# Kernel tuning notes

Measured on AMD Instinct MI355X. Metric: run time of the kernel, lower is better.

## Reference

```python
import jax, jax.numpy as jnp
import numpy as np

B, HIMG, WIMG = 8, 24, 24
WIDTH, NCH, CW = 1024, 8, 128
NHEADS, HD = 8, 16
HALF = HD // 2
NFREQ, VOCAB, NCLS = 32, 256, 10
HIDDEN = 4096
EPS = 1e-6
LAMBDA_INIT = 0.8 - 0.6 * float(np.exp(-0.3 * 0.0))  # layer_idx = 0


def rmsnorm(x, w, eps=EPS):
    return x * jax.lax.rsqrt(jnp.mean(x * x, axis=-1, keepdims=True) + eps) * w


def causal_attn(q, k, v, scale):
    # q,k: [B,H,L,d2], v: [B,H,L,D]
    L = q.shape[2]
    scores = jnp.einsum('bhqd,bhkd->bhqk', q, k) * scale
    mask = jnp.tril(jnp.ones((L, L), dtype=bool))
    scores = jnp.where(mask, scores, -jnp.inf)
    return jnp.einsum('bhqk,bhkd->bhqd', jax.nn.softmax(scores, axis=-1), v)


def diff_attn(h, qkv_w, qkv_b, qn_w, kn_w, hn_w, lq1, lk1, lq2, lk2, ow, ob):
    Bb, L, C = h.shape
    qkv = jax.nn.silu(h @ qkv_w + qkv_b).reshape(Bb, L, 3, NHEADS, HD)
    q, k, v = qkv[:, :, 0], qkv[:, :, 1], qkv[:, :, 2]
    t = lambda a: a.transpose(0, 2, 1, 3)  # [B,L,H,d] -> [B,H,L,d]
    q1 = t(rmsnorm(q[..., :HALF], qn_w)); q2 = t(rmsnorm(q[..., HALF:], qn_w))
    k1 = t(rmsnorm(k[..., :HALF], kn_w)); k2 = t(rmsnorm(k[..., HALF:], kn_w))
    v = t(v)
    lam = jnp.exp(jnp.dot(lq1, lk1)) - jnp.exp(jnp.dot(lq2, lk2)) + LAMBDA_INIT
    scale = 1.0 / np.sqrt(HALF)
    out1 = causal_attn(q1, k1, v, scale)
    out2 = causal_attn(q2, k2, v, scale)
    diff = rmsnorm(out1 - lam * out2, hn_w) * (1.0 - LAMBDA_INIT)
    out = diff.transpose(0, 2, 1, 3).reshape(Bb, L, C)
    return jax.nn.silu(out @ ow + ob)


def setup_inputs() -> dict:
    key = jax.random.key(0)
    ks = iter(jax.random.split(key, 64))
    n = lambda shape, s=0.02: jax.random.normal(next(ks), shape, jnp.float32) * s
    return dict(
        x=jax.random.uniform(next(ks), (B, HIMG, WIMG), jnp.float32),
        top_k=4,
        pixel_embed=n((VOCAB, WIDTH)),
        freq_h=n((NFREQ,), 0.1), freq_w=n((NFREQ,), 0.1),
        phase_h=jnp.zeros((NFREQ,), jnp.float32), phase_w=jnp.zeros((NFREQ,), jnp.float32),
        pos_proj_w=n((4 * NFREQ, WIDTH)), pos_proj_b=jnp.zeros((WIDTH,), jnp.float32),
        embed_norm_w=jnp.ones((WIDTH,), jnp.float32),
        se_w1=n((WIDTH, WIDTH // 4)), se_b1=jnp.zeros((WIDTH // 4,), jnp.float32),
        se_w2=n((WIDTH // 4, WIDTH)), se_b2=jnp.zeros((WIDTH,), jnp.float32),
        mix_norm_w=jnp.ones((WIDTH,), jnp.float32),
        mlp_w1=n((WIDTH, HIDDEN)), mlp_b1=jnp.zeros((HIDDEN,), jnp.float32),
        mlp_w2=n((HIDDEN, WIDTH)), mlp_b2=jnp.zeros((WIDTH,), jnp.float32),
        mlp_norm_w=jnp.ones((WIDTH,), jnp.float32),
        router_w=n((WIDTH, NCH)), router_b=jnp.zeros((NCH,), jnp.float32),
        qkv_w=n((NCH, CW, 3 * CW)), qkv_b=jnp.zeros((NCH, 3 * CW), jnp.float32),
        q_norm_w=jnp.ones((NCH, HALF), jnp.float32), k_norm_w=jnp.ones((NCH, HALF), jnp.float32),
        head_norm_w=jnp.ones((NCH, HD), jnp.float32),
        lam_q1=n((NCH, HALF), 0.1), lam_k1=n((NCH, HALF), 0.1),
        lam_q2=n((NCH, HALF), 0.1), lam_k2=n((NCH, HALF), 0.1),
        out_w=n((NCH, CW, CW)), out_b=jnp.zeros((NCH, CW), jnp.float32),
        seg_norm_w=jnp.ones((NCH, CW), jnp.float32),
        head_w=n((WIDTH, NCLS)), head_b=jnp.zeros((NCLS,), jnp.float32),
    )


def reference(x, top_k, pixel_embed, freq_h, freq_w, phase_h, phase_w, pos_proj_w,
              pos_proj_b, embed_norm_w, se_w1, se_b1, se_w2, se_b2, mix_norm_w,
              mlp_w1, mlp_b1, mlp_w2, mlp_b2, mlp_norm_w, router_w, router_b,
              qkv_w, qkv_b, q_norm_w, k_norm_w, head_norm_w, lam_q1, lam_k1,
              lam_q2, lam_k2, out_w, out_b, seg_norm_w, head_w, head_b):
    Bb, H, W = x.shape
    L = H * W
    # LearnedSinusoidal2DEmbed
    hp = jnp.arange(H, dtype=jnp.float32) / H
    wp = jnp.arange(W, dtype=jnp.float32) / W
    fh = jax.nn.softplus(freq_h) * 10.0
    fw = jax.nn.softplus(freq_w) * 10.0
    ha = hp[:, None] * fh + phase_h          # [H, NFREQ]
    wa = wp[:, None] * fw + phase_w
    h_enc = jnp.concatenate([jnp.sin(ha), jnp.cos(ha)], -1)
    w_enc = jnp.concatenate([jnp.sin(wa), jnp.cos(wa)], -1)
    pos = jnp.concatenate([jnp.broadcast_to(h_enc[:, None], (H, W, 2 * NFREQ)),
                           jnp.broadcast_to(w_enc[None, :], (H, W, 2 * NFREQ))], -1)
    pos = pos @ pos_proj_w + pos_proj_b      # [H, W, WIDTH]
    xi = jnp.clip((x * 255.0).astype(jnp.int32), 0, 255).reshape(Bb, L)
    h = pixel_embed[xi] + pos.reshape(1, L, WIDTH)
    h = rmsnorm(h, embed_norm_w)
    # ChannelMixer: SE + RMSNorm residual, MLP residual, top-k router
    s = jnp.mean(h, axis=1)
    s = jax.nn.sigmoid(jax.nn.silu(s @ se_w1 + se_b1) @ se_w2 + se_b2)
    h = h + rmsnorm(h * s[:, None, :] - h, mix_norm_w)
    h = h + rmsnorm(jax.nn.silu(h @ mlp_w1 + mlp_b1) @ mlp_w2 + mlp_b2, mlp_norm_w)
    logits_r = jnp.mean(h, axis=1) @ router_w + router_b   # [B, NCH]
    tv, ti = jax.lax.top_k(logits_r, top_k)
    rw = jnp.zeros_like(logits_r).at[jnp.arange(Bb)[:, None], ti].set(jax.nn.softmax(tv, axis=-1))
    # ChannelSegment: per-channel differential attention expert, routed
    outs = []
    for i in range(NCH):
        hi = h[..., i * CW:(i + 1) * CW]
        o = diff_attn(hi, qkv_w[i], qkv_b[i], q_norm_w[i], k_norm_w[i], head_norm_w[i],
                      lam_q1[i], lam_k1[i], lam_q2[i], lam_k2[i], out_w[i], out_b[i])
        hi = hi + rmsnorm(o, seg_norm_w[i])
        outs.append(hi * rw[:, i][:, None, None])
    h = jnp.concatenate(outs, axis=-1)
    # classifier head
    return jnp.mean(h, axis=1) @ head_w + head_b
```

## Files before the change

### kernel.cpp

```cpp
#include <hip/hip_runtime.h>
#include <math.h>

typedef __bf16 bf16;
typedef __bf16 bf16x8 __attribute__((ext_vector_type(8)));
typedef __bf16 bf16x4 __attribute__((ext_vector_type(4)));
typedef __bf16 bf16x2 __attribute__((ext_vector_type(2)));
typedef float f32x4 __attribute__((ext_vector_type(4)));
typedef short s16x4 __attribute__((ext_vector_type(4)));

constexpr int Bsz = 8, HIMG = 24, WIMG = 24;
constexpr int Lq = 576;
constexpr int WIDTH = 1024, NCH = 8, CW = 128;
constexpr int NHEADS = 8, HD = 16, HALF = 8;
constexpr float EPS = 1e-6f;
constexpr float LAMINIT = 0.2f;
constexpr float QSCALE_E = 0.35355339059327373f * 1.4426950408889634f;
constexpr int ROWS = Bsz * Lq;
constexpr long PSTRIDE = 4718592;

__device__ __forceinline__ float fexp2(float x) {
#if __has_builtin(__builtin_amdgcn_exp2f)
  return __builtin_amdgcn_exp2f(x);
#else
  return exp2f(x);
#endif
}

constexpr size_t B_HB    = 0;
constexpr size_t B_G2B   = B_HB    + 9437184;
constexpr size_t B_ENCB  = B_G2B   + 9437184;
constexpr size_t B_POSWT = B_ENCB  + 163840;
constexpr size_t B_QKVWT = B_POSWT + 262144;
constexpr size_t B_OWT   = B_QKVWT + 786432;
constexpr size_t B_SE    = B_OWT   + 262144;
constexpr size_t B_T1    = B_SE    + 32768;
constexpr size_t B_MP    = B_T1    + 8192;
constexpr size_t B_RW    = B_MP    + 524288;
constexpr size_t B_LAM   = B_RW    + 256;
constexpr size_t B_POOL  = B_LAM   + 256;
constexpr size_t WS_BIG  = B_POOL + 8388608 + 8388608 + 37748736;
constexpr size_t WS_BIG2 = WS_BIG + 9437184;
constexpr size_t WS_BIG3 = WS_BIG + 4 * 9437184;

__device__ __forceinline__ float blockReduceSum256(float v, float* red) {
  #pragma unroll
  for (int off = 32; off; off >>= 1) v += __shfl_down(v, off, 64);
  int lane = threadIdx.x & 63, wid = threadIdx.x >> 6;
  if (lane == 0) red[wid] = v;
  __syncthreads();
  float total = 0.f;
  #pragma unroll
  for (int i = 0; i < 4; i++) total += red[i];
  return total;
}
__device__ __forceinline__ float silu(float x) { return x / (1.f + __expf(-x)); }

__device__ __forceinline__ void gl16(const bf16* g, bf16* l) {
  __builtin_amdgcn_global_load_lds(
      (const __attribute__((address_space(1))) void*)g,
      (__attribute__((address_space(3))) void*)l, 16, 0, 0);
}

__device__ __forceinline__ f32x4 mfma16(bf16x4 a, bf16x4 b, f32x4 c) {
#if __has_builtin(__builtin_amdgcn_mfma_f32_16x16x16bf16_1k)
  union { bf16x4 h; s16x4 s; } ua, ub;
  ua.h = a; ub.h = b;
  return __builtin_amdgcn_mfma_f32_16x16x16bf16_1k(ua.s, ub.s, c, 0, 0, 0);
#else
  f32x4 d = c;
  asm volatile("v_mfma_f32_16x16x16_bf16 %0, %1, %2, %0"
               : "+v"(d) : "v"(a), "v"(b));
  return d;
#endif
}

__device__ __forceinline__ void tcast_tile(const float* __restrict__ W,
    bf16* __restrict__ Wt, int K, int N, long zo, int bx, int by) {
  __shared__ float t[32][33];
  int n0 = bx * 32, k0 = by * 32;
  int tid = threadIdx.x;
  int r = tid >> 3, c4 = (tid & 7) * 4;
  const float4 v = *(const float4*)(W + zo + (long)(k0 + r) * N + n0 + c4);
  t[c4 + 0][r] = v.x; t[c4 + 1][r] = v.y; t[c4 + 2][r] = v.z; t[c4 + 3][r] = v.w;
  __syncthreads();
  bf16* dst = Wt + zo + (long)(n0 + r) * K + k0 + c4;
  bf16x4 o4;
  o4[0] = (bf16)t[r][c4 + 0]; o4[1] = (bf16)t[r][c4 + 1];
  o4[2] = (bf16)t[r][c4 + 2]; o4[3] = (bf16)t[r][c4 + 3];
  *(bf16x4*)dst = o4;
}

__global__ __launch_bounds__(256) void k_tcast_all(
    const float* __restrict__ w1, const float* __restrict__ w2,
    const float* __restrict__ posw, const float* __restrict__ qkvw,
    const float* __restrict__ outw,
    bf16* __restrict__ W1T, bf16* __restrict__ W2T, bf16* __restrict__ POSWT,
    bf16* __restrict__ QKVWT, bf16* __restrict__ OWT) {
  int bid = blockIdx.x;
  if (bid < 4096) {
    tcast_tile(w1, W1T, 1024, 4096, 0, bid % 128, bid / 128);
  } else if (bid < 8192) {
    int t = bid - 4096;
    tcast_tile(w2, W2T, 4096, 1024, 0, t % 32, t / 32);
  } else if (bid < 8320) {
    int t = bid - 8192;
    tcast_tile(posw, POSWT, 128, 1024, 0, t % 32, t / 32);
  } else if (bid < 8704) {
    int t = bid - 8320;
    int z = t / 48; t -= z * 48;
    tcast_tile(qkvw, QKVWT, 128, 384, (long)z * 49152, t % 12, t / 12);
  } else {
    int t = bid - 8704;
    int z = t / 16; t -= z * 16;
    tcast_tile(outw, OWT, 128, 128, (long)z * 16384, t % 4, t / 4);
  }
}

__global__ void k_enc_b(const float* __restrict__ fh, const float* __restrict__ fw,
                        const float* __restrict__ ph, const float* __restrict__ pw,
                        bf16* __restrict__ enc) {
  int idx = blockIdx.x * blockDim.x + threadIdx.x;
  if (idx >= Lq * 128) return;
  int l = idx >> 7, c = idx & 127;
  int hh = l / WIMG, ww = l % WIMG;
  float v;
  if (c < 64) {
    int f = c & 31;
    float fr = log1pf(__expf(fh[f])) * 10.f;
    float a = (hh / (float)HIMG) * fr + ph[f];
    v = (c < 32) ? sinf(a) : cosf(a);
  } else {
    int f = c & 31;
    float fr = log1pf(__expf(fw[f])) * 10.f;
    float a = (ww / (float)WIMG) * fr + pw[f];
    v = (c < 96) ? sinf(a) : cosf(a);
  }
  enc[idx] = (bf16)v;
}

template <int ACT, int OUTBF, int SWZ>
__global__ __launch_bounds__(256) void gemm_bt(
    const bf16* __restrict__ A, int lda, long aZs,
    const bf16* __restrict__ Bt, int ldb, long bZs,
    const float* __restrict__ bias, int biasZs,
    void* __restrict__ Cv, int ldc, long cZs,
    int M, int N, int K) {
  __shared__ bf16 As[128 * 32];
  __shared__ bf16 Bs[128 * 32];
  int tid = threadIdx.x;
  int m0, n0, z;
  if constexpr (SWZ == 0) {
    m0 = blockIdx.y * 128; n0 = blockIdx.x * 128; z = blockIdx.z;
  } else if constexpr (SWZ == 1) {
    int lid = blockIdx.x;
    int xcd = lid & 7, idx = lid >> 3;
    int j = idx & 15, G = xcd + 8 * (idx >> 4);
    m0 = (G % 36) * 128; n0 = ((G / 36) * 16 + j) * 128; z = 0;
  } else {
    int lid = blockIdx.x;
    int xcd = lid & 7, idx = lid >> 3;
    int n = idx & 7, G = xcd + 8 * (idx >> 3);
    m0 = (G % 36) * 128; n0 = n * 128; z = G / 36;
  }
  const bf16* Ab = A + (long)z * aZs;
  const bf16* Bb = Bt + (long)z * bZs;
  f32x4 acc[4][4] = {};
  int wv = tid >> 6, lane = tid & 63;
  int wrow = (wv >> 1) * 64, wcol = (wv & 1) * 64;
  int lm = lane & 15, lq = lane >> 4;
  const bf16* ag = Ab + (long)(m0 + (tid >> 2)) * lda + (tid & 3) * 8;
  const bf16* bg = Bb + (long)(n0 + (tid >> 2)) * ldb + (tid & 3) * 8;
  bf16* asd = As + tid * 8;
  bf16* bsd = Bs + tid * 8;
  for (int k0 = 0; k0 < K; k0 += 32) {
    gl16(ag + k0, asd);
    gl16(ag + k0 + 64L * lda, asd + 2048);
    gl16(bg + k0, bsd);
    gl16(bg + k0 + 64L * ldb, bsd + 2048);
    __syncthreads();
    bf16x8 af[4], bfr[4];
    #pragma unroll
    for (int i = 0; i < 4; i++) {
      af[i]  = *(const bf16x8*)(As + (wrow + i * 16 + lm) * 32 + lq * 8);
      bfr[i] = *(const bf16x8*)(Bs + (wcol + i * 16 + lm) * 32 + lq * 8);
    }
    #pragma unroll
    for (int i = 0; i < 4; i++)
      #pragma unroll
      for (int j = 0; j < 4; j++)
        acc[i][j] = __builtin_amdgcn_mfma_f32_16x16x32_bf16(af[i], bfr[j], acc[i][j], 0, 0, 0);
    __syncthreads();
  }
  long cz = (long)z * cZs;
  const float* bz = bias ? bias + (long)z * biasZs : nullptr;
  #pragma unroll
  for (int i = 0; i < 4; i++) {
    int row = m0 + wrow + i * 16 + lq * 4;
    #pragma unroll
    for (int j = 0; j < 4; j++) {
      int col = n0 + wcol + j * 16 + lm;
      float bv = bz ? bz[col] : 0.f;
      #pragma unroll
      for (int r = 0; r < 4; r++) {
        float v = acc[i][j][r] + bv;
        if (ACT == 1) v = silu(v);
        long off = cz + (long)(row + r) * ldc + col;
        if (OUTBF) ((bf16*)Cv)[off] = (bf16)v;
        else       ((float*)Cv)[off] = v;
      }
    }
  }
}

template <int ACT>
__global__ __launch_bounds__(512) void gemm256(
    const bf16* __restrict__ A, int lda, long aZs,
    const bf16* __restrict__ Bt, int ldb, long bZs,
    const float* __restrict__ bias,
    bf16* __restrict__ C, int ldc, long cZs,
    int Mtiles, int Ntiles, int K) {
  __shared__ bf16 LDS[65536];
  const int tid = threadIdx.x;
  const int cpx = gridDim.x >> 3;
  const int wg = (blockIdx.x & 7) * cpx + (blockIdx.x >> 3);
  const int per_z = Mtiles * Ntiles;
  const int z = wg / per_z, rwg = wg % per_z;
  const int m0 = (rwg / Ntiles) * 256, n0 = (rwg % Ntiles) * 256;
  const bf16* Ab = A + (long)z * aZs;
  const bf16* Bb = Bt + (long)z * bZs;
  const int c0 = tid, c1 = tid + 512;
  const int sr0 = c0 >> 3, sc0 = ((c0 & 7) ^ (((sr0 >> 2) & 1) << 1)) * 8;
  const int sr1 = c1 >> 3, sc1 = ((c1 & 7) ^ (((sr1 >> 2) & 1) << 1)) * 8;
  const long a00 = (long)(m0 + sr0) * lda + sc0;
  const long a01 = (long)(m0 + sr1) * lda + sc1;
  const long a10 = (long)(m0 + 128 + sr0) * lda + sc0;
  const long a11 = (long)(m0 + 128 + sr1) * lda + sc1;
  const long b00 = (long)(n0 + sr0) * ldb + sc0;
  const long b01 = (long)(n0 + sr1) * ldb + sc1;
  const long b10 = (long)(n0 + 128 + sr0) * ldb + sc0;
  const long b11 = (long)(n0 + 128 + sr1) * ldb + sc1;
  const int d0 = c0 * 8, d1 = c1 * 8;
  auto stage = [&](int kt, int buf) {
    const bf16* Ak = Ab + kt * 64;
    const bf16* Bk = Bb + kt * 64;
    bf16* L = LDS + buf * 32768;
    gl16(Ak + a00, L + d0);         gl16(Ak + a01, L + d1);
    gl16(Ak + a10, L + 8192 + d0);  gl16(Ak + a11, L + 8192 + d1);
    gl16(Bk + b00, L + 16384 + d0); gl16(Bk + b01, L + 16384 + d1);
    gl16(Bk + b10, L + 24576 + d0); gl16(Bk + b11, L + 24576 + d1);
  };
  const int wv = tid >> 6, lane = tid & 63;
  const int wm = wv >> 2, wn = wv & 3;
  const int lm = lane & 15, lq = lane >> 4;
  const int swb = ((lm >> 2) & 1) << 1;
  const int abase = wm * 8192;
  const int bbase = 16384 + (wn >> 1) * 8192;
  const int brow0 = (wn & 1) * 64;
  const int kq0 = (lq ^ swb) * 8;
  const int kq1 = ((4 + lq) ^ swb) * 8;
  f32x4 acc[8][4] = {};
  bf16x8 afr[4][2], bfr[2][2];
  const int NT = K >> 6;
  stage(0, 0);
  asm volatile("s_waitcnt vmcnt(0)" ::: "memory");
  __builtin_amdgcn_s_barrier();
  for (int s = 0; s < NT; ++s) {
    const int bb = (s & 1) * 32768;
    const bf16* La = LDS + bb + abase + lm * 64;
    const bf16* Lb = LDS + bb + bbase + (brow0 + lm) * 64;
    #pragma unroll
    for (int f = 0; f < 4; f++) {
      afr[f][0] = *(const bf16x8*)(La + f * 1024 + kq0);
      afr[f][1] = *(const bf16x8*)(La + f * 1024 + kq1);
    }
    #pragma unroll
    for (int g = 0; g < 2; g++) {
      bfr[g][0] = *(const bf16x8*)(Lb + g * 1024 + kq0);
      bfr[g][1] = *(const bf16x8*)(Lb + g * 1024 + kq1);
    }
    if (s + 1 < NT) stage(s + 1, ((s & 1) ^ 1));
    __builtin_amdgcn_s_barrier();
    __builtin_amdgcn_s_setprio(1);
    #pragma unroll
    for (int f = 0; f < 4; f++)
      #pragma unroll
      for (int g = 0; g < 2; g++) {
        acc[f][g] = __builtin_amdgcn_mfma_f32_16x16x32_bf16(afr[f][0], bfr[g][0], acc[f][g], 0, 0, 0);
        acc[f][g] = __builtin_amdgcn_mfma_f32_16x16x32_bf16(afr[f][1], bfr[g][1], acc[f][g], 0, 0, 0);
      }
    __builtin_amdgcn_s_setprio(0);
    __builtin_amdgcn_s_barrier();
    #pragma unroll
    for (int g = 0; g < 2; g++) {
      bfr[g][0] = *(const bf16x8*)(Lb + 2048 + g * 1024 + kq0);
      bfr[g][1] = *(const bf16x8*)(Lb + 2048 + g * 1024 + kq1);
    }
    __builtin_amdgcn_s_barrier();
    __builtin_amdgcn_s_setprio(1);
    #pragma unroll
    for (int f = 0; f < 4; f++)
      #pragma unroll
      for (int g = 0; g < 2; g++) {
        acc[f][2 + g] = __builtin_amdgcn_mfma_f32_16x16x32_bf16(afr[f][0], bfr[g][0], acc[f][2 + g], 0, 0, 0);
        acc[f][2 + g] = __builtin_amdgcn_mfma_f32_16x16x32_bf16(afr[f][1], bfr[g][1], acc[f][2 + g], 0, 0, 0);
      }
    __builtin_amdgcn_s_setprio(0);
    __builtin_amdgcn_s_barrier();
    #pragma unroll
    for (int f = 0; f < 4; f++) {
      afr[f][0] = *(const bf16x8*)(La + 4096 + f * 1024 + kq0);
      afr[f][1] = *(const bf16x8*)(La + 4096 + f * 1024 + kq1);
    }
    __builtin_amdgcn_s_barrier();
    __builtin_amdgcn_s_setprio(1);
    #pragma unroll
    for (int f = 0; f < 4; f++)
      #pragma unroll
      for (int g = 0; g < 2; g++) {
        acc[4 + f][2 + g] = __builtin_amdgcn_mfma_f32_16x16x32_bf16(afr[f][0], bfr[g][0], acc[4 + f][2 + g], 0, 0, 0);
        acc[4 + f][2 + g] = __builtin_amdgcn_mfma_f32_16x16x32_bf16(afr[f][1], bfr[g][1], acc[4 + f][2 + g], 0, 0, 0);
      }
    __builtin_amdgcn_s_setprio(0);
    __builtin_amdgcn_s_barrier();
    #pragma unroll
    for (int g = 0; g < 2; g++) {
      bfr[g][0] = *(const bf16x8*)(Lb + g * 1024 + kq0);
      bfr[g][1] = *(const bf16x8*)(Lb + g * 1024 + kq1);
    }
    __builtin_amdgcn_s_barrier();
    __builtin_amdgcn_s_setprio(1);
    #pragma unroll
    for (int f = 0; f < 4; f++)
      #pragma unroll
      for (int g = 0; g < 2; g++) {
        acc[4 + f][g] = __builtin_amdgcn_mfma_f32_16x16x32_bf16(afr[f][0], bfr[g][0], acc[4 + f][g], 0, 0, 0);
        acc[4 + f][g] = __builtin_amdgcn_mfma_f32_16x16x32_bf16(afr[f][1], bfr[g][1], acc[4 + f][g], 0, 0, 0);
      }
    __builtin_amdgcn_s_setprio(0);
    if (s + 1 < NT) { asm volatile("s_waitcnt vmcnt(0)" ::: "memory"); }
    __builtin_amdgcn_s_barrier();
  }
  const long cz = (long)z * cZs;
  #pragma unroll
  for (int i = 0; i < 8; i++) {
    const int row = m0 + wm * 128 + (i >> 2) * 64 + (i & 3) * 16 + lq * 4;
    #pragma unroll
    for (int j = 0; j < 4; j++) {
      const int col = n0 + wn * 64 + (j >> 1) * 32 + (j & 1) * 16 + lm;
      const float bv = bias ? bias[col] : 0.f;
      #pragma unroll
      for (int rr = 0; rr < 4; rr++) {
        float v = acc[i][j][rr] + bv;
        if (ACT == 1) v = silu(v);
        C[cz + (long)(row + rr) * ldc + col] = (bf16)v;
      }
    }
  }
}

template <int ACT, int OUTBF, int ACC, int NORM>
__global__ __launch_bounds__(256) void gemm64(
    const bf16* __restrict__ A, int lda, long aZs,
    const bf16* __restrict__ Bt, int ldb, long bZs,
    const float* __restrict__ bias, int biasZs,
    void* __restrict__ Cv, int ldc, long cZs,
    int M, int N, int K,
    const float* __restrict__ qn, const float* __restrict__ kn) {
  __shared__ bf16 As[64 * 32];
  __shared__ bf16 Bs[128 * 32];
  int tid = threadIdx.x;
  int m0 = blockIdx.y * 64, n0 = blockIdx.x * 128;
  int z = blockIdx.z;
  const bf16* Ab = A + (long)z * aZs;
  const bf16* Bb = Bt + (long)z * bZs;
  f32x4 acc[4][2] = {};
  int wv = tid >> 6, lane = tid & 63;
  int lm = lane & 15, lq = lane >> 4;
  int wcol = wv * 32;
  const bf16* ag = Ab + (long)(m0 + (tid >> 2)) * lda + (tid & 3) * 8;
  const bf16* bg = Bb + (long)(n0 + (tid >> 2)) * ldb + (tid & 3) * 8;
  bf16* asd = As + tid * 8;
  bf16* bsd = Bs + tid * 8;
  for (int k0 = 0; k0 < K; k0 += 32) {
    gl16(ag + k0, asd);
    gl16(bg + k0, bsd);
    gl16(bg + k0 + 64L * ldb, bsd + 2048);
    __syncthreads();
    bf16x8 af[4], bfr[2];
    #pragma unroll
    for (int i = 0; i < 4; i++)
      af[i] = *(const bf16x8*)(As + (i * 16 + lm) * 32 + lq * 8);
    #pragma unroll
    for (int j = 0; j < 2; j++)
      bfr[j] = *(const bf16x8*)(Bs + (wcol + j * 16 + lm) * 32 + lq * 8);
    #pragma unroll
    for (int i = 0; i < 4; i++)
      #pragma unroll
      for (int j = 0; j < 2; j++)
        acc[i][j] = __builtin_amdgcn_mfma_f32_16x16x32_bf16(af[i], bfr[j], acc[i][j], 0, 0, 0);
    __syncthreads();
  }
  long cz = (long)z * cZs;
  const float* bz = bias ? bias + (long)z * biasZs : nullptr;
  if constexpr (NORM == 0) {
    #pragma unroll
    for (int i = 0; i < 4; i++) {
      int row = m0 + i * 16 + lq * 4;
      #pragma unroll
      for (int j = 0; j < 2; j++) {
        int col = n0 + wcol + j * 16 + lm;
        float bv = bz ? bz[col] : 0.f;
        #pragma unroll
        for (int r = 0; r < 4; r++) {
          float v = acc[i][j][r] + bv;
          long off = cz + (long)(row + r) * ldc + col;
          if (ACC) v += (float)((bf16*)Cv)[off];
          if (ACT == 1) v = silu(v);
          if (OUTBF) ((bf16*)Cv)[off] = (bf16)v;
          else       ((float*)Cv)[off] = v;
        }
      }
    }
  } else {
    int nsec = blockIdx.x;
    bool don = nsec < 2;
    float wnv = 1.f;
    if (nsec == 0) wnv = qn[z * 8 + (lm & 7)] * QSCALE_E;
    else if (nsec == 1) wnv = kn[z * 8 + (lm & 7)];
    #pragma unroll
    for (int i = 0; i < 4; i++) {
      int row = m0 + i * 16 + lq * 4;
      #pragma unroll
      for (int j = 0; j < 2; j++) {
        int col = n0 + wcol + j * 16 + lm;
        float bv = bz ? bz[col] : 0.f;
        #pragma unroll
        for (int r = 0; r < 4; r++) {
          float v = acc[i][j][r] + bv;
          if (ACT == 1) v = silu(v);
          float s = v * v;
          s += __shfl_xor(s, 1);
          s += __shfl_xor(s, 2);
          s += __shfl_xor(s, 4);
          if (don) v = v * rsqrtf(s * 0.125f + EPS) * wnv;
          ((bf16*)Cv)[cz + (long)(row + r) * ldc + col] = (bf16)v;
        }
      }
    }
  }
}

__global__ __launch_bounds__(256) void k_embed(const float* __restrict__ x,
    const float* __restrict__ emb, const float* __restrict__ pos,
    const float* __restrict__ nw, bf16* __restrict__ h) {
  __shared__ float red[4];
  int row = blockIdx.x;
  int l = row % Lq;
  int xi = (int)(x[row] * 255.f);
  xi = min(max(xi, 0), 255);
  const float* er = emb + (long)xi * WIDTH;
  const float* pr = pos + (long)l * WIDTH;
  int c0 = threadIdx.x * 4;
  float v[4]; float ss = 0.f;
  #pragma unroll
  for (int i = 0; i < 4; i++) { v[i] = er[c0 + i] + pr[c0 + i]; ss += v[i] * v[i]; }
  ss = blockReduceSum256(ss, red);
  float r = rsqrtf(ss / WIDTH + EPS);
  bf16* hr = h + (long)row * WIDTH;
  #pragma unroll
  for (int i = 0; i < 4; i++) hr[c0 + i] = (bf16)(v[i] * r * nw[c0 + i]);
}

__global__ void k_meanl_p(const bf16* __restrict__ h, float* __restrict__ part) {
  int lp = blockIdx.x, b = blockIdx.y, t = threadIdx.x;
  const bf16* p = h + ((long)b * Lq + (long)lp * 36) * WIDTH + t * 4;
  float a0 = 0, a1 = 0, a2 = 0, a3 = 0;
  for (int l = 0; l < 36; l++) {
    bf16x4 v = *(const bf16x4*)(p + (long)l * WIDTH);
    a0 += (float)v[0]; a1 += (float)v[1]; a2 += (float)v[2]; a3 += (float)v[3];
  }
  float* dst = part + ((long)b * 16 + lp) * WIDTH + t * 4;
  dst[0] = a0; dst[1] = a1; dst[2] = a2; dst[3] = a3;
}

__global__ __launch_bounds__(256) void k_se1(const float* __restrict__ part,
    const float* __restrict__ w1, const float* __restrict__ b1,
    float* __restrict__ t1) {
  __shared__ float sv[1024];
  __shared__ float red[256];
  int jb = blockIdx.x, b = blockIdx.y, t = threadIdx.x;
  for (int c = t; c < 1024; c += 256) {
    float a = 0.f;
    #pragma unroll
    for (int lp = 0; lp < 16; lp++) a += part[((long)b * 16 + lp) * 1024 + c];
    sv[c] = a * (1.f / 576.f);
  }
  __syncthreads();
  int j = t & 7, pt = t >> 3;
  int j0 = jb * 8;
  float acc = 0.f;
  int c0 = pt * 32;
  #pragma unroll 8
  for (int c = c0; c < c0 + 32; c++) acc += sv[c] * w1[c * 256 + j0 + j];
  red[t] = acc;
  __syncthreads();
  if (t < 8) {
    float a = b1[j0 + t];
    #pragma unroll
    for (int p = 0; p < 32; p++) a += red[p * 8 + t];
    t1[b * 256 + j0 + t] = silu(a);
  }
}

__global__ __launch_bounds__(256) void k_se2(const float* __restrict__ t1,
    const float* __restrict__ w2, const float* __restrict__ b2,
    float* __restrict__ s) {
  __shared__ float red[256];
  int jb = blockIdx.x, b = blockIdx.y, t = threadIdx.x;
  int j = t & 31, pt = t >> 5;
  int j0 = jb * 32;
  const float* tb = t1 + b * 256;
  float acc = 0.f;
  int c0 = pt * 32;
  #pragma unroll 8
  for (int c = c0; c < c0 + 32; c++) acc += tb[c] * w2[c * 1024 + j0 + j];
  red[t] = acc;
  __syncthreads();
  if (t < 32) {
    float a = b2[j0 + t];
    #pragma unroll
    for (int p = 0; p < 8; p++) a += red[p * 32 + t];
    s[b * 1024 + j0 + t] = 1.f / (1.f + __expf(-a));
  }
}

__global__ __launch_bounds__(256) void k_mix_b(bf16* __restrict__ h,
    const float* __restrict__ s, const float* __restrict__ mw) {
  __shared__ float red[4];
  int row = blockIdx.x;
  int b = row / Lq;
  bf16* hr = h + (long)row * WIDTH;
  const float* sb = s + b * WIDTH;
  int c0 = threadIdx.x * 4;
  float hv[4], y[4]; float ss = 0.f;
  #pragma unroll
  for (int i = 0; i < 4; i++) {
    hv[i] = (float)hr[c0 + i];
    y[i] = hv[i] * (sb[c0 + i] - 1.f); ss += y[i] * y[i];
  }
  ss = blockReduceSum256(ss, red);
  float r = rsqrtf(ss / WIDTH + EPS);
  #pragma unroll
  for (int i = 0; i < 4; i++) hr[c0 + i] = (bf16)(hv[i] + y[i] * r * mw[c0 + i]);
}

__global__ __launch_bounds__(256) void k_addnorm_b(bf16* __restrict__ h,
    const bf16* __restrict__ g, const float* __restrict__ mw) {
  __shared__ float red[4];
  int row = blockIdx.x;
  bf16* hr = h + (long)row * WIDTH;
  const bf16* gr = g + (long)row * WIDTH;
  int c0 = threadIdx.x * 4;
  float y[4]; float ss = 0.f;
  #pragma unroll
  for (int i = 0; i < 4; i++) { y[i] = (float)gr[c0 + i]; ss += y[i] * y[i]; }
  ss = blockReduceSum256(ss, red);
  float r = rsqrtf(ss / WIDTH + EPS);
  #pragma unroll
  for (int i = 0; i < 4; i++)
    hr[c0 + i] = (bf16)((float)hr[c0 + i] + y[i] * r * mw[c0 + i]);
}

__global__ __launch_bounds__(256) void k_addnorm2(bf16* __restrict__ h,
    const bf16* __restrict__ p0, const bf16* __restrict__ p1,
    const float* __restrict__ b2, const float* __restrict__ mw) {
  __shared__ float red[4];
  int row = blockIdx.x;
  bf16* hr = h + (long)row * WIDTH;
  const bf16* g0 = p0 + (long)row * WIDTH;
  const bf16* g1 = p1 + (long)row * WIDTH;
  int c0 = threadIdx.x * 4;
  float y[4]; float ss = 0.f;
  #pragma unroll
  for (int i = 0; i < 4; i++) {
    y[i] = (float)g0[c0 + i] + (float)g1[c0 + i] + b2[c0 + i];
    ss += y[i] * y[i];
  }
  ss = blockReduceSum256(ss, red);
  float r = rsqrtf(ss / WIDTH + EPS);
  #pragma unroll
  for (int i = 0; i < 4; i++)
    hr[c0 + i] = (bf16)((float)hr[c0 + i] + y[i] * r * mw[c0 + i]);
}

__global__ __launch_bounds__(256) void k_addnorm4(bf16* __restrict__ h,
    const bf16* __restrict__ parts, const float* __restrict__ b2,
    const float* __restrict__ mw) {
  __shared__ float red[4];
  int row = blockIdx.x;
  bf16* hr = h + (long)row * WIDTH;
  const bf16* g0 = parts + (long)row * WIDTH;
  int c0 = threadIdx.x * 4;
  float y[4]; float ss = 0.f;
  #pragma unroll
  for (int i = 0; i < 4; i++) {
    float a = b2[c0 + i];
    #pragma unroll
    for (int p = 0; p < 4; p++) a += (float)g0[(long)p * PSTRIDE + c0 + i];
    y[i] = a; ss += a * a;
  }
  ss = blockReduceSum256(ss, red);
  float r = rsqrtf(ss / WIDTH + EPS);
  #pragma unroll
  for (int i = 0; i < 4; i++)
    hr[c0 + i] = (bf16)((float)hr[c0 + i] + y[i] * r * mw[c0 + i]);
}

__global__ __launch_bounds__(256) void k_router(const float* __restrict__ part,
    const float* __restrict__ rwgt, const float* __restrict__ rb,
    const float* __restrict__ lq1, const float* __restrict__ lk1,
    const float* __restrict__ lq2, const float* __restrict__ lk2,
    float* __restrict__ rw, float* __restrict__ lam) {
  __shared__ float sv[1024];
  __shared__ float red[256];
  __shared__ float lg[8];
  int b = blockIdx.x, t = threadIdx.x;
  for (int c = t; c < 1024; c += 256) {
    float a = 0.f;
    #pragma unroll
    for (int lp = 0; lp < 16; lp++) a += part[((long)b * 16 + lp) * 1024 + c];
    sv[c] = a * (1.f / 576.f);
  }
  __syncthreads();
  int j = t & 7, pt = t >> 3;
  float acc = 0.f;
  int c0 = pt * 32;
  #pragma unroll 8
  for (int c = c0; c < c0 + 32; c++) acc += sv[c] * rwgt[c * 8 + j];
  red[t] = acc;
  __syncthreads();
  if (t < 8) {
    float a = rb[t];
    for (int p = 0; p < 32; p++) a += red[p * 8 + t];
    lg[t] = a;
  }
  __syncthreads();
  if (t == 0) {
    float v[8]; bool sel[8];
    #pragma unroll
    for (int i = 0; i < 8; i++) { v[i] = lg[i]; sel[i] = false; }
    int idxs[4]; float vals[4];
    for (int s = 0; s < 4; s++) {
      int bi = -1; float bv = -1e30f;
      for (int i = 0; i < 8; i++) if (!sel[i] && v[i] > bv) { bv = v[i]; bi = i; }
      sel[bi] = true; idxs[s] = bi; vals[s] = bv;
    }
    float m = vals[0], den = 0.f, e[4];
    for (int s = 0; s < 4; s++) { e[s] = __expf(vals[s] - m); den += e[s]; }
    for (int i = 0; i < 8; i++) rw[b * 8 + i] = 0.f;
    for (int s = 0; s < 4; s++) rw[b * 8 + idxs[s]] = e[s] / den;
  }
  if (b == 0 && t >= 8 && t < 16) {
    int c = t - 8;
    float d1 = 0.f, d2 = 0.f;
    for (int i = 0; i < 8; i++) {
      d1 += lq1[c * 8 + i] * lk1[c * 8 + i];
      d2 += lq2[c * 8 + i] * lk2[c * 8 + i];
    }
    lam[c] = __expf(d1) - __expf(d2) + LAMINIT;
  }
}

__global__ __launch_bounds__(256) void k_attn_mfma(
    const bf16* __restrict__ qkv, const float* __restrict__ lam,
    const float* __restrict__ hnw, bf16* __restrict__ dc) {
  __shared__ bf16 Ks[576 * 16];
  __shared__ bf16 Vt[16 * 584];
  int tid = threadIdx.x;
  int slice = blockIdx.x; int zc = slice >> 3, b = slice & 7;
  int head = blockIdx.z;
  const bf16* qkvb = qkv + ((long)zc * ROWS + (long)b * Lq) * 384;
  for (int i = tid; i < 1152; i += 256) {
    int row = i >> 1, hf = i & 1;
    gl16(qkvb + (long)row * 384 + 128 + head * 16 + hf * 8, Ks + i * 8);
  }
  for (int i = tid; i < 1152; i += 256) {
    int row = i >> 1, dh = i & 1;
    bf16x8 v = *(const bf16x8*)(qkvb + (long)row * 384 + 256 + head * 16 + dh * 8);
    #pragma unroll
    for (int j = 0; j < 8; j++) Vt[(dh * 8 + j) * 584 + row] = v[j];
  }
  __syncthreads();
  int wv = tid >> 6, lane = tid & 63;
  int lm = lane & 15, lq = lane >> 4;
  float lamv = lam[zc];
  float hwv[4];
  #pragma unroll
  for (int r = 0; r < 4; r++) hwv[r] = hnw[zc * 16 + lq * 4 + r] * (1.f - LAMINIT);
  const bf16 one = (bf16)1.0f;
  const bf16x4 ONES = {one, one, one, one};
  int u = blockIdx.y * 4 + wv;
  int prA, prB, prC;
  if (u < 6) { prA = u + 2; prB = 17 - u; prC = -1; }
  else       { int v2 = u - 6; prA = v2; prB = 8 + v2; prC = 11 - v2; }
  for (int pi = 0; pi < 3; pi++) {
    int pr = (pi == 0) ? prA : (pi == 1) ? prB : prC;
    if (pr < 0) continue;
    bf16x8 bq0[2] = {{}, {}}, bq1[2] = {{}, {}};
    if (lq < 2) {
      #pragma unroll
      for (int tile = 0; tile < 2; tile++) {
        bf16x8 t8 = *(const bf16x8*)(
            qkvb + (long)(pr * 32 + tile * 16 + lm) * 384 + head * 16 + lq * 8);
        if (lq == 0) bq0[tile] = t8; else bq1[tile] = t8;
      }
    }
    f32x4 o[2][2] = {};
    f32x4 dacc[2][2] = {};
    for (int kc = 0; kc <= pr; kc++) {
      f32x4 sT[2][2][2] = {};
      #pragma unroll
      for (int t = 0; t < 2; t++) {
        bf16x8 aK = {};
        if (lq < 2) aK = *(const bf16x8*)(Ks + (kc * 32 + t * 16 + lm) * 16 + lq * 8);
        #pragma unroll
        for (int tile = 0; tile < 2; tile++) {
          sT[t][tile][0] = __builtin_amdgcn_mfma_f32_16x16x32_bf16(aK, bq0[tile], sT[t][tile][0], 0, 0, 0);
          sT[t][tile][1] = __builtin_amdgcn_mfma_f32_16x16x32_bf16(aK, bq1[tile], sT[t][tile][1], 0, 0, 0);
        }
      }
      bool diag = (kc == pr);
      #pragma unroll
      for (int t = 0; t < 2; t++) {
        bf16x4 aV = *(const bf16x4*)(Vt + lm * 584 + kc * 32 + t * 16 + lq * 4);
        #pragma unroll
        for (int tile = 0; tile < 2; tile++) {
          if (diag && tile == 0 && t == 1) continue;
          bool masked = diag && (tile == t);
          #pragma unroll
          for (int h2 = 0; h2 < 2; h2++) {
            bf16x4 pb;
            #pragma unroll
            for (int r = 0; r < 4; r++) {
              float ev = fexp2(sT[t][tile][h2][r]);
              if (masked && (lq * 4 + r > lm)) ev = 0.f;
              pb[r] = (bf16)ev;
            }
            dacc[tile][h2] = mfma16(ONES, pb, dacc[tile][h2]);
            o[tile][h2] = mfma16(aV, pb, o[tile][h2]);
          }
        }
      }
    }
    #pragma unroll
    for (int tile = 0; tile < 2; tile++) {
      float inv1 = 1.f / dacc[tile][0][0];
      float inv2 = lamv / dacc[tile][1][0];
      float dff[4]; float ss = 0.f;
      #pragma unroll
      for (int r = 0; r < 4; r++) {
        dff[r] = o[tile][0][r] * inv1 - o[tile][1][r] * inv2;
        ss += dff[r] * dff[r];
      }
      ss += __shfl_xor(ss, 16);
      ss += __shfl_xor(ss, 32);
      float rr = rsqrtf(ss * 0.0625f + EPS);
      bf16x4 outp;
      #pragma unroll
      for (int r = 0; r < 4; r++) outp[r] = (bf16)(dff[r] * rr * hwv[r]);
      long rowg = (long)zc * ROWS + (long)b * Lq + pr * 32 + tile * 16 + lm;
      *(bf16x4*)(dc + rowg * 128 + head * 16 + lq * 4) = outp;
    }
  }
}

__global__ __launch_bounds__(64) void k_segpool(const bf16* __restrict__ h,
    const bf16* __restrict__ op, const float* __restrict__ segw,
    const float* __restrict__ rw, float* __restrict__ part) {
  int lp = blockIdx.x, b = blockIdx.y, ch = blockIdx.z;
  int t = threadIdx.x;
  int c0 = t * 2;
  float w0 = segw[ch * 128 + c0], w1 = segw[ch * 128 + c0 + 1];
  float rwv = rw[b * 8 + ch];
  float a0 = 0.f, a1 = 0.f;
  for (int l = 0; l < 36; l++) {
    int row = b * Lq + lp * 36 + l;
    const bf16* oprow = op + (long)ch * ROWS * CW + (long)row * CW;
    bf16x2 yv = *(const bf16x2*)(oprow + c0);
    float y0 = (float)yv[0], y1 = (float)yv[1];
    float ss = y0 * y0 + y1 * y1;
    #pragma unroll
    for (int m = 1; m < 64; m <<= 1) ss += __shfl_xor(ss, m);
    float r = rsqrtf(ss * (1.f / 128.f) + EPS);
    bf16x2 hv = *(const bf16x2*)(h + (long)row * WIDTH + ch * 128 + c0);
    a0 += ((float)hv[0] + y0 * r * w0) * rwv;
    a1 += ((float)hv[1] + y1 * r * w1) * rwv;
  }
  float* dst = part + ((long)b * 16 + lp) * 1024 + ch * 128 + c0;
  dst[0] = a0; dst[1] = a1;
}

__global__ __launch_bounds__(256) void k_head(const float* __restrict__ part,
    const float* __restrict__ hw, const float* __restrict__ hb, float* __restrict__ out) {
  __shared__ float pool[1024];
  __shared__ float red[256];
  int b = blockIdx.x, t = threadIdx.x;
  for (int c = t; c < 1024; c += 256) {
    float a = 0.f;
    #pragma unroll
    for (int lp = 0; lp < 16; lp++) a += part[((long)b * 16 + lp) * 1024 + c];
    pool[c] = a * (1.f / 576.f);
  }
  __syncthreads();
  int j = t & 15, pt = t >> 4;
  float acc = 0.f;
  if (j < 10)
    for (int c = pt * 64; c < pt * 64 + 64; c++)
      acc += pool[c] * hw[c * 10 + j];
  red[t] = acc;
  __syncthreads();
  if (t < 10) {
    float a = hb[t];
    for (int p = 0; p < 16; p++) a += red[p * 16 + t];
    out[b * 10 + t] = a;
  }
}

extern "C" void kernel_launch(void* const* d_in, const int* in_sizes, int n_in,
                              void* d_out, int out_size, void* d_ws, size_t ws_size,
                              hipStream_t stream) {
  const float* x          = (const float*)d_in[0];
  const float* pixel_embed= (const float*)d_in[2];
  const float* freq_h     = (const float*)d_in[3];
  const float* freq_w     = (const float*)d_in[4];
  const float* phase_h    = (const float*)d_in[5];
  const float* phase_w    = (const float*)d_in[6];
  const float* pos_proj_w = (const float*)d_in[7];
  const float* pos_proj_b = (const float*)d_in[8];
  const float* embed_norm = (const float*)d_in[9];
  const float* se_w1      = (const float*)d_in[10];
  const float* se_b1      = (const float*)d_in[11];
  const float* se_w2      = (const float*)d_in[12];
  const float* se_b2      = (const float*)d_in[13];
  const float* mix_norm   = (const float*)d_in[14];
  const float* mlp_w1     = (const float*)d_in[15];
  const float* mlp_b1     = (const float*)d_in[16];
  const float* mlp_w2     = (const float*)d_in[17];
  const float* mlp_b2     = (const float*)d_in[18];
  const float* mlp_norm   = (const float*)d_in[19];
  const float* router_w   = (const float*)d_in[20];
  const float* router_b   = (const float*)d_in[21];
  const float* qkv_w      = (const float*)d_in[22];
  const float* qkv_b      = (const float*)d_in[23];
  const float* q_norm_w   = (const float*)d_in[24];
  const float* k_norm_w   = (const float*)d_in[25];
  const float* head_norm_w= (const float*)d_in[26];
  const float* lam_q1     = (const float*)d_in[27];
  const float* lam_k1     = (const float*)d_in[28];
  const float* lam_q2     = (const float*)d_in[29];
  const float* lam_k2     = (const float*)d_in[30];
  const float* out_w      = (const float*)d_in[31];
  const float* out_b      = (const float*)d_in[32];
  const float* seg_norm_w = (const float*)d_in[33];
  const float* head_w     = (const float*)d_in[34];
  const float* head_b     = (const float*)d_in[35];

  char* W = (char*)d_ws;
  bf16*  HB    = (bf16*)(W + B_HB);
  bf16*  G2B   = (bf16*)(W + B_G2B);
  float* POS   = (float*)(W + B_G2B);
  bf16*  ENCB  = (bf16*)(W + B_ENCB);
  bf16*  POSWT = (bf16*)(W + B_POSWT);
  bf16*  QKVWT = (bf16*)(W + B_QKVWT);
  bf16*  OWT   = (bf16*)(W + B_OWT);
  float* SE    = (float*)(W + B_SE);
  float* T1    = (float*)(W + B_T1);
  float* MP    = (float*)(W + B_MP);
  float* RW    = (float*)(W + B_RW);
  float* LAM   = (float*)(W + B_LAM);
  char*  P     = W + B_POOL;
  bf16*  W1T   = (bf16*)P;
  bf16*  W2T   = (bf16*)(P + 8388608);
  bf16*  HID   = (bf16*)(P + 16777216);
  bf16*  PARTS = (bf16*)(P + 16777216 + 37748736);
  bf16*  QKV   = (bf16*)P;
  bf16*  DC    = (bf16*)(P + 28311552);
  float* out   = (float*)d_out;
  const int tier = (ws_size >= WS_BIG3) ? 3 : (ws_size >= WS_BIG2) ? 2
                 : (ws_size >= WS_BIG) ? 1 : 0;

  k_tcast_all<<<8832, 256, 0, stream>>>(mlp_w1, mlp_w2, pos_proj_w, qkv_w, out_w,
                                        W1T, W2T, POSWT, QKVWT, OWT);
  k_enc_b<<<288, 256, 0, stream>>>(freq_h, freq_w, phase_h, phase_w, ENCB);
  gemm64<0, 0, 0, 0><<<dim3(8, 10, 1), 256, 0, stream>>>(
      ENCB, 128, 0, POSWT, 128, 0, pos_proj_b, 0, POS, 1024, 0, 640, 1024, 128,
      nullptr, nullptr);
  k_embed<<<ROWS, 256, 0, stream>>>(x, pixel_embed, POS, embed_norm, HB);
  k_meanl_p<<<dim3(16, 8), 256, 0, stream>>>(HB, MP);
  k_se1<<<dim3(32, 8), 256, 0, stream>>>(MP, se_w1, se_b1, T1);
  k_se2<<<dim3(32, 8), 256, 0, stream>>>(T1, se_w2, se_b2, SE);
  k_mix_b<<<ROWS, 256, 0, stream>>>(HB, SE, mix_norm);
  if (tier >= 1) {
    gemm256<1><<<256, 512, 0, stream>>>(
        HB, 1024, 0, W1T, 1024, 0, mlp_b1,
        HID, 4096, 0, 16, 16, 1024);
    gemm_bt<1, 1, 0><<<dim3(32, 4, 1), 256, 0, stream>>>(
        HB + 4096L * 1024, 1024, 0, W1T, 1024, 0, mlp_b1, 0,
        HID + 4096L * 4096, 4096, 0, 512, 4096, 1024);
    if (tier == 3) {
      gemm256<0><<<256, 512, 0, stream>>>(
          HID, 4096, 1024, W2T, 4096, 1024, nullptr,
          PARTS, 1024, PSTRIDE, 16, 4, 1024);
      gemm_bt<0, 1, 0><<<dim3(8, 4, 4), 256, 0, stream>>>(
          HID + 4096L * 4096, 4096, 1024, W2T, 4096, 1024, nullptr, 0,
          PARTS + 4096L * 1024, 1024, PSTRIDE, 512, 1024, 1024);
      k_addnorm4<<<ROWS, 256, 0, stream>>>(HB, PARTS, mlp_b2, mlp_norm);
    } else if (tier == 2) {
      gemm_bt<0, 1, 2><<<576, 256, 0, stream>>>(
          HID, 4096, 2048, W2T, 4096, 2048, nullptr, 0,
          G2B, 1024, (long)(PARTS - G2B), 4608, 1024, 2048);
      k_addnorm2<<<ROWS, 256, 0, stream>>>(HB, G2B, PARTS, mlp_b2, mlp_norm);
    } else {
      gemm64<0, 1, 0, 0><<<dim3(8, 72, 1), 256, 0, stream>>>(
          HID, 4096, 0, W2T, 4096, 0, mlp_b2, 0,
          G2B, 1024, 0, 4608, 1024, 4096, nullptr, nullptr);
      k_addnorm_b<<<ROWS, 256, 0, stream>>>(HB, G2B, mlp_norm);
    }
  } else {
    gemm_bt<1, 1, 0><<<dim3(16, 36, 1), 256, 0, stream>>>(
        HB, 1024, 0, W1T, 1024, 0, mlp_b1, 0, HID, 2048, 0, 4608, 2048, 1024);
    gemm64<0, 1, 0, 0><<<dim3(8, 72, 1), 256, 0, stream>>>(
        HID, 2048, 0, W2T, 4096, 0, mlp_b2, 0, G2B, 1024, 0, 4608, 1024, 2048,
        nullptr, nullptr);
    gemm_bt<1, 1, 0><<<dim3(16, 36, 1), 256, 0, stream>>>(
        HB, 1024, 0, W1T + 2048L * 1024, 1024, 0, mlp_b1 + 2048, 0, HID, 2048, 0,
        4608, 2048, 1024);
    gemm64<0, 1, 1, 0><<<dim3(8, 72, 1), 256, 0, stream>>>(
        HID, 2048, 0, W2T + 2048, 4096, 0, nullptr, 0, G2B, 1024, 0,
        4608, 1024, 2048, nullptr, nullptr);
    k_addnorm_b<<<ROWS, 256, 0, stream>>>(HB, G2B, mlp_norm);
  }
  k_meanl_p<<<dim3(16, 8), 256, 0, stream>>>(HB, MP);
  k_router<<<8, 256, 0, stream>>>(MP, router_w, router_b,
                                  lam_q1, lam_k1, lam_q2, lam_k2, RW, LAM);
  gemm64<1, 1, 0, 1><<<dim3(3, 72, 8), 256, 0, stream>>>(
      HB, 1024, CW, QKVWT, 128, 384 * 128, qkv_b, 384,
      QKV, 384, (long)ROWS * 384, ROWS, 384, 128, q_norm_w, k_norm_w);
  k_attn_mfma<<<dim3(64, 2, 8), 256, 0, stream>>>(QKV, LAM, head_norm_w, DC);
  gemm64<1, 1, 0, 0><<<dim3(1, 72, 8), 256, 0, stream>>>(
      DC, 128, (long)ROWS * 128, OWT, 128, 128 * 128, out_b, 128,
      DC, 128, (long)ROWS * 128, ROWS, 128, 128, nullptr, nullptr);
  k_segpool<<<dim3(16, 8, 8), 64, 0, stream>>>(HB, DC, seg_norm_w, RW, MP);
  k_head<<<8, 256, 0, stream>>>(MP, head_w, head_b, out);
}
```

Before: 456.2 us.

## Use full XOR LDS swizzle and drop intra-iteration barriers in gemm256

The LDS swizzle now XORs the 16-byte column chunk with the full row index (row & 7) instead of a single bit, aiming to spread fragment reads across more banks. The main loop now uses one __syncthreads per K-step and issues the next stage's global-to-LDS loads right after it. All A and B fragments for the step are held in separate registers, so the eight s_barrier calls between MFMA groups are gone. The cost is more VGPRs per thread, which may limit occupancy or cause spills. It also relies on __syncthreads draining the outstanding async LDS loads.

```diff
diff --git a/kernel.cpp b/kernel.cpp
--- a/kernel.cpp
+++ b/kernel.cpp
@@ -229,8 +229,8 @@
   const bf16* Ab = A + (long)z * aZs;
   const bf16* Bb = Bt + (long)z * bZs;
   const int c0 = tid, c1 = tid + 512;
-  const int sr0 = c0 >> 3, sc0 = ((c0 & 7) ^ (((sr0 >> 2) & 1) << 1)) * 8;
-  const int sr1 = c1 >> 3, sc1 = ((c1 & 7) ^ (((sr1 >> 2) & 1) << 1)) * 8;
+  const int sr0 = c0 >> 3, sc0 = ((c0 & 7) ^ (sr0 & 7)) * 8;
+  const int sr1 = c1 >> 3, sc1 = ((c1 & 7) ^ (sr1 & 7)) * 8;
   const long a00 = (long)(m0 + sr0) * lda + sc0;
   const long a01 = (long)(m0 + sr1) * lda + sc1;
   const long a10 = (long)(m0 + 128 + sr0) * lda + sc0;
@@ -252,93 +252,78 @@
   const int wv = tid >> 6, lane = tid & 63;
   const int wm = wv >> 2, wn = wv & 3;
   const int lm = lane & 15, lq = lane >> 4;
-  const int swb = ((lm >> 2) & 1) << 1;
+  const int sw = lm & 7;
   const int abase = wm * 8192;
   const int bbase = 16384 + (wn >> 1) * 8192;
   const int brow0 = (wn & 1) * 64;
-  const int kq0 = (lq ^ swb) * 8;
-  const int kq1 = ((4 + lq) ^ swb) * 8;
+  const int kq0 = (lq ^ sw) * 8;
+  const int kq1 = ((4 + lq) ^ sw) * 8;
   f32x4 acc[8][4] = {};
-  bf16x8 afr[4][2], bfr[2][2];
   const int NT = K >> 6;
   stage(0, 0);
-  asm volatile("s_waitcnt vmcnt(0)" ::: "memory");
-  __builtin_amdgcn_s_barrier();
   for (int s = 0; s < NT; ++s) {
+    __syncthreads();
+    if (s + 1 < NT) stage(s + 1, (s + 1) & 1);
     const int bb = (s & 1) * 32768;
     const bf16* La = LDS + bb + abase + lm * 64;
     const bf16* Lb = LDS + bb + bbase + (brow0 + lm) * 64;
+    bf16x8 a0[4][2], a1[4][2], b0[2][2], b1[2][2];
     #pragma unroll
     for (int f = 0; f < 4; f++) {
-      afr[f][0] = *(const bf16x8*)(La + f * 1024 + kq0);
-      afr[f][1] = *(const bf16x8*)(La + f * 1024 + kq1);
+      a0[f][0] = *(const bf16x8*)(La + f * 1024 + kq0);
+      a0[f][1] = *(const bf16x8*)(La + f * 1024 + kq1);
     }
     #pragma unroll
     for (int g = 0; g < 2; g++) {
-      bfr[g][0] = *(const bf16x8*)(Lb + g * 1024 + kq0);
-      bfr[g][1] = *(const bf16x8*)(Lb + g * 1024 + kq1);
-    }
-    if (s + 1 < NT) stage(s + 1, ((s & 1) ^ 1));
-    __builtin_amdgcn_s_barrier();
+      b0[g][0] = *(const bf16x8*)(Lb + g * 1024 + kq0);
+      b0[g][1] = *(const bf16x8*)(Lb + g * 1024 + kq1);
+    }
     __builtin_amdgcn_s_setprio(1);
     #pragma unroll
     for (int f = 0; f < 4; f++)
       #pragma unroll
       for (int g = 0; g < 2; g++) {
-        acc[f][g] = __builtin_amdgcn_mfma_f32_16x16x32_bf16(afr[f][0], bfr[g][0], acc[f][g], 0, 0, 0);
-        acc[f][g] = __builtin_amdgcn_mfma_f32_16x16x32_bf16(afr[f][1], bfr[g][1], acc[f][g], 0, 0, 0);
+        acc[f][g] = __builtin_amdgcn_mfma_f32_16x16x32_bf16(a0[f][0], b0[g][0], acc[f][g], 0, 0, 0);
+        acc[f][g] = __builtin_amdgcn_mfma_f32_16x16x32_bf16(a0[f][1], b0[g][1], acc[f][g], 0, 0, 0);
       }
     __builtin_amdgcn_s_setprio(0);
-    __builtin_amdgcn_s_barrier();
     #pragma unroll
     for (int g = 0; g < 2; g++) {
-      bfr[g][0] = *(const bf16x8*)(Lb + 2048 + g * 1024 + kq0);
-      bfr[g][1] = *(const bf16x8*)(Lb + 2048 + g * 1024 + kq1);
-    }
-    __builtin_amdgcn_s_barrier();
+      b1[g][0] = *(const bf16x8*)(Lb + 2048 + g * 1024 + kq0);
+      b1[g][1] = *(const bf16x8*)(Lb + 2048 + g * 1024 + kq1);
+    }
     __builtin_amdgcn_s_setprio(1);
     #pragma unroll
     for (int f = 0; f < 4; f++)
       #pragma unroll
       for (int g = 0; g < 2; g++) {
-        acc[f][2 + g] = __builtin_amdgcn_mfma_f32_16x16x32_bf16(afr[f][0], bfr[g][0], acc[f][2 + g], 0, 0, 0);
-        acc[f][2 + g] = __builtin_amdgcn_mfma_f32_16x16x32_bf16(afr[f][1], bfr[g][1], acc[f][2 + g], 0, 0, 0);
+        acc[f][2 + g] = __builtin_amdgcn_mfma_f32_16x16x32_bf16(a0[f][0], b1[g][0], acc[f][2 + g], 0, 0, 0);
+        acc[f][2 + g] = __builtin_amdgcn_mfma_f32_16x16x32_bf16(a0[f][1], b1[g][1], acc[f][2 + g], 0, 0, 0);
       }
     __builtin_amdgcn_s_setprio(0);
-    __builtin_amdgcn_s_barrier();
     #pragma unroll
     for (int f = 0; f < 4; f++) {
-      afr[f][0] = *(const bf16x8*)(La + 4096 + f * 1024 + kq0);
-      afr[f][1] = *(const bf16x8*)(La + 4096 + f * 1024 + kq1);
-    }
-    __builtin_amdgcn_s_barrier();
+      a1[f][0] = *(const bf16x8*)(La + 4096 + f * 1024 + kq0);
+      a1[f][1] = *(const bf16x8*)(La + 4096 + f * 1024 + kq1);
+    }
     __builtin_amdgcn_s_setprio(1);
     #pragma unroll
     for (int f = 0; f < 4; f++)
       #pragma unroll
       for (int g = 0; g < 2; g++) {
-        acc[4 + f][2 + g] = __builtin_amdgcn_mfma_f32_16x16x32_bf16(afr[f][0], bfr[g][0], acc[4 + f][2 + g], 0, 0, 0);
-        acc[4 + f][2 + g] = __builtin_amdgcn_mfma_f32_16x16x32_bf16(afr[f][1], bfr[g][1], acc[4 + f][2 + g], 0, 0, 0);
+        acc[4 + f][2 + g] = __builtin_amdgcn_mfma_f32_16x16x32_bf16(a1[f][0], b1[g][0], acc[4 + f][2 + g], 0, 0, 0);
+        acc[4 + f][2 + g] = __builtin_amdgcn_mfma_f32_16x16x32_bf16(a1[f][1], b1[g][1], acc[4 + f][2 + g], 0, 0, 0);
       }
     __builtin_amdgcn_s_setprio(0);
-    __builtin_amdgcn_s_barrier();
-    #pragma unroll
-    for (int g = 0; g < 2; g++) {
-      bfr[g][0] = *(const bf16x8*)(Lb + g * 1024 + kq0);
-      bfr[g][1] = *(const bf16x8*)(Lb + g * 1024 + kq1);
-    }
-    __builtin_amdgcn_s_barrier();
     __builtin_amdgcn_s_setprio(1);
     #pragma unroll
     for (int f = 0; f < 4; f++)
       #pragma unroll
       for (int g = 0; g < 2; g++) {
-        acc[4 + f][g] = __builtin_amdgcn_mfma_f32_16x16x32_bf16(afr[f][0], bfr[g][0], acc[4 + f][g], 0, 0, 0);
-        acc[4 + f][g] = __builtin_amdgcn_mfma_f32_16x16x32_bf16(afr[f][1], bfr[g][1], acc[4 + f][g], 0, 0, 0);
+        acc[4 + f][g] = __builtin_amdgcn_mfma_f32_16x16x32_bf16(a1[f][0], b0[g][0], acc[4 + f][g], 0, 0, 0);
+        acc[4 + f][g] = __builtin_amdgcn_mfma_f32_16x16x32_bf16(a1[f][1], b0[g][1], acc[4 + f][g], 0, 0, 0);
       }
     __builtin_amdgcn_s_setprio(0);
-    if (s + 1 < NT) { asm volatile("s_waitcnt vmcnt(0)" ::: "memory"); }
-    __builtin_amdgcn_s_barrier();
   }
   const long cz = (long)z * cZs;
   #pragma unroll
```

Measured after the change: 437.7 us. 4.1% less time.
